# Optimization experiments

Measured on AMD Instinct MI355X. Metric: run time of the kernel, lower is better.

Reference implementation:

```python
import jax, jax.numpy as jnp
import numpy as np

N_NODES = 100000
N_EDGES = 1600000
IN_FEATS = 128
N_HIDDEN = 128
N_CLASSES = 47


def setup_inputs() -> dict:
    key = jax.random.key(0)
    ks = jax.random.split(key, 9)
    x = jax.random.normal(ks[0], (N_NODES, IN_FEATS), dtype=jnp.float32)
    src = jax.random.randint(ks[1], (N_EDGES,), 0, N_NODES, dtype=jnp.int32)
    dst = jax.random.randint(ks[2], (N_EDGES,), 0, N_NODES, dtype=jnp.int32)
    s = 0.05
    return {
        "x": x, "src": src, "dst": dst,
        "Ws0": jax.random.normal(ks[3], (IN_FEATS, N_HIDDEN), jnp.float32) * s,
        "Wn0": jax.random.normal(ks[4], (IN_FEATS, N_HIDDEN), jnp.float32) * s,
        "b0": jnp.zeros((N_HIDDEN,), jnp.float32),
        "Ws1": jax.random.normal(ks[5], (N_HIDDEN, N_HIDDEN), jnp.float32) * s,
        "Wn1": jax.random.normal(ks[6], (N_HIDDEN, N_HIDDEN), jnp.float32) * s,
        "b1": jnp.zeros((N_HIDDEN,), jnp.float32),
        "Ws2": jax.random.normal(ks[7], (N_HIDDEN, N_CLASSES), jnp.float32) * s,
        "Wn2": jax.random.normal(ks[8], (N_HIDDEN, N_CLASSES), jnp.float32) * s,
        "b2": jnp.zeros((N_CLASSES,), jnp.float32),
    }


def _sage_layer(h, src, dst, inv_deg, Ws, Wn, b):
    # weighted (w=1) mean aggregation over in-neighbors: sum(h[src]) / in_degree
    msg = h[src]  # [E, d] irregular gather
    neigh = jax.ops.segment_sum(msg, dst, num_segments=N_NODES) * inv_deg[:, None]
    # DGL SAGEConv 'mean': fc_self(h_self) + fc_neigh(h_neigh), bias on self branch
    return h @ Ws + neigh @ Wn + b


def reference(x, src, dst, Ws0, Wn0, b0, Ws1, Wn1, b1, Ws2, Wn2, b2):
    deg = jax.ops.segment_sum(jnp.ones_like(dst, dtype=x.dtype), dst, num_segments=N_NODES)
    inv_deg = 1.0 / jnp.maximum(deg, 1.0)
    h = _sage_layer(x, src, dst, inv_deg, Ws0, Wn0, b0)
    h = jax.nn.relu(h)  # dropout is identity (eval / p=0)
    h = _sage_layer(h, src, dst, inv_deg, Ws1, Wn1, b1)
    h = jax.nn.relu(h)
    h = _sage_layer(h, src, dst, inv_deg, Ws2, Wn2, b2)
    return jax.nn.log_softmax(h, axis=-1)
```

## Files before the change

### kernel.cpp

```cpp
#include <hip/hip_runtime.h>
#include <hip/hip_bf16.h>

#define NN 100000
#define NE 1600000
#define F 128
#define NCLS 47

#define NPB 256
#define BUCKETS 391
#define ABLK 512
#define ACHUNK (NE / ABLK)

typedef __attribute__((ext_vector_type(8))) short short8;
typedef __attribute__((ext_vector_type(8))) unsigned short u16x8;
typedef __attribute__((ext_vector_type(4))) float f32x4;

#define MFMA16(A, B, C) __builtin_amdgcn_mfma_f32_16x16x32_bf16(A, B, C, 0, 0, 0)

__device__ __forceinline__ unsigned short b16(float f) {
    unsigned int u = __builtin_bit_cast(unsigned int, f);
    unsigned int r = u + 0x7FFFu + ((u >> 16) & 1u);
    return (unsigned short)(r >> 16);
}
__device__ __forceinline__ float bflo(unsigned int u) { return __builtin_bit_cast(float, u << 16); }
__device__ __forceinline__ float bfhi(unsigned int u) { return __builtin_bit_cast(float, u & 0xFFFF0000u); }

__global__ void __launch_bounds__(256) k_bhist(const int* __restrict__ dst,
                                               int* __restrict__ bucket_cnt) {
    __shared__ int hist[BUCKETS];
    const int t = threadIdx.x;
    for (int i = t; i < BUCKETS; i += 256) hist[i] = 0;
    __syncthreads();
    const int e0 = blockIdx.x * ACHUNK;
    for (int i = t; i < ACHUNK; i += 256) atomicAdd(&hist[dst[e0 + i] >> 8], 1);
    __syncthreads();
    for (int i = t; i < BUCKETS; i += 256)
        if (hist[i]) atomicAdd(&bucket_cnt[i], hist[i]);
}

__global__ void k_bscan(const int* __restrict__ bucket_cnt, int* __restrict__ bucket_off,
                        int* __restrict__ cursor) {
    const int lane = threadIdx.x & 63;
    int run = 0;
#pragma unroll
    for (int c = 0; c < 7; c++) {
        int idx = c * 64 + lane;
        int v = (idx < BUCKETS) ? bucket_cnt[idx] : 0;
        int s = v;
#pragma unroll
        for (int off = 1; off < 64; off <<= 1) {
            int n = __shfl_up(s, off);
            if (lane >= off) s += n;
        }
        int excl = run + s - v;
        if (idx <= BUCKETS) {
            bucket_off[idx] = excl;
            cursor[idx] = excl;
        }
        run += __shfl(s, 63);
    }
}

__global__ void __launch_bounds__(256) k_bscatter(const int* __restrict__ src,
                                                  const int* __restrict__ dst,
                                                  int* __restrict__ cursor,
                                                  int2* __restrict__ ebuf) {
    __shared__ int hist[BUCKETS];
    __shared__ int base[BUCKETS];
    __shared__ int rank[BUCKETS];
    const int t = threadIdx.x;
    for (int i = t; i < BUCKETS; i += 256) {
        hist[i] = 0;
        rank[i] = 0;
    }
    __syncthreads();
    const int e0 = blockIdx.x * ACHUNK;
    for (int i = t; i < ACHUNK; i += 256) atomicAdd(&hist[dst[e0 + i] >> 8], 1);
    __syncthreads();
    for (int i = t; i < BUCKETS; i += 256) {
        int h = hist[i];
        base[i] = h ? atomicAdd(&cursor[i], h) : 0;
    }
    __syncthreads();
    for (int i = t; i < ACHUNK; i += 256) {
        int s = src[e0 + i];
        int d = dst[e0 + i];
        int b = d >> 8;
        int r = atomicAdd(&rank[b], 1);
        ebuf[base[b] + r] = make_int2(s, d);
    }
}

__global__ void __launch_bounds__(256) k_bcsr(const int2* __restrict__ ebuf,
                                              const int* __restrict__ bucket_off,
                                              int* __restrict__ row_off,
                                              float* __restrict__ inv_deg,
                                              int* __restrict__ col) {
    __shared__ int cnt[NPB];
    __shared__ int ro[NPB];
    __shared__ int wsum[4];
    const int t = threadIdx.x, lane = t & 63, wid = t >> 6;
    cnt[t] = 0;
    __syncthreads();
    const int e0 = bucket_off[blockIdx.x], e1 = bucket_off[blockIdx.x + 1];
    for (int i = e0 + t; i < e1; i += 256) atomicAdd(&cnt[ebuf[i].y & 255], 1);
    __syncthreads();
    int v = cnt[t];
    int run = v;
#pragma unroll
    for (int off = 1; off < 64; off <<= 1) {
        int n = __shfl_up(run, off);
        if (lane >= off) run += n;
    }
    if (lane == 63) wsum[wid] = run;
    __syncthreads();
    int woff = e0;
#pragma unroll
    for (int wv = 0; wv < 4; wv++)
        if (wv < wid) woff += wsum[wv];
    int excl = woff + run - v;
    int node = (blockIdx.x << 8) + t;
    if (node < NN) {
        row_off[node] = excl;
        inv_deg[node] = 1.0f / fmaxf((float)v, 1.0f);
    }
    if (blockIdx.x == BUCKETS - 1 && t == 0) row_off[NN] = NE;
    ro[t] = excl;
    cnt[t] = 0;
    __syncthreads();
    for (int i = e0 + t; i < e1; i += 256) {
        int2 e = ebuf[i];
        int d = e.y & 255;
        int p = atomicAdd(&cnt[d], 1);
        col[ro[d] + p] = e.x;
    }
}

__global__ void k_cvt(const float* __restrict__ x, unsigned short* __restrict__ xb) {
    int t = blockIdx.x * blockDim.x + threadIdx.x;
    if (t >= NN * F / 8) return;
    const float4* x4 = (const float4*)x;
    float4 a = x4[t * 2], b = x4[t * 2 + 1];
    u16x8 o;
    o[0] = b16(a.x); o[1] = b16(a.y); o[2] = b16(a.z); o[3] = b16(a.w);
    o[4] = b16(b.x); o[5] = b16(b.y); o[6] = b16(b.z); o[7] = b16(b.w);
    ((u16x8*)xb)[t] = o;
}

__global__ void k_zpad(unsigned short* __restrict__ xb, unsigned short* __restrict__ h1b,
                       unsigned short* __restrict__ hw2b) {
    int t = threadIdx.x;
    xb[(size_t)NN * F + t] = 0;
    h1b[(size_t)NN * F + t] = 0;
    if (t < 64) hw2b[(size_t)NN * 64 + t] = 0;
}

__global__ void k_pack_all(const float* __restrict__ Ws0, const float* __restrict__ Wn0,
                           const float* __restrict__ Ws1, const float* __restrict__ Wn1,
                           const float* __restrict__ Ws2, const float* __restrict__ Wn2,
                           unsigned short* __restrict__ wp) {
    int idx = blockIdx.x * blockDim.x + threadIdx.x;
    if (idx >= 77824) return;
    const float* W;
    int base, ncols;
    if (idx < 65536) {
        int m = idx >> 14;
        W = (m == 0) ? Ws0 : (m == 1) ? Wn0 : (m == 2) ? Ws1 : Wn1;
        base = m << 14;
        ncols = 128;
    } else {
        int m = (idx - 65536) / 6144;
        W = m ? Wn2 : Ws2;
        base = 65536 + m * 6144;
        ncols = NCLS;
    }
    int li = idx - base;
    int nt = li >> 11;
    int r = li & 2047;
    int kk = r >> 9;
    int r2 = r & 511;
    int lane = r2 >> 3;
    int j = r2 & 7;
    int k = kk * 32 + ((lane >> 4) << 3) + j;
    int n = nt * 16 + (lane & 15);
    float v = (n < ncols) ? W[k * ncols + n] : 0.f;
    wp[idx] = b16(v);
}

__global__ void __launch_bounds__(256) k_aggb(const uint4* __restrict__ h4,
                                              const int* __restrict__ row_off,
                                              const int* __restrict__ col,
                                              const float* __restrict__ inv_deg,
                                              uint4* __restrict__ a4) {
    int node = (blockIdx.x * blockDim.x + threadIdx.x) >> 6;
    int lane = threadIdx.x & 63;
    if (node >= NN) return;
    int b = row_off[node], e = row_off[node + 1];
    int deg = e - b;
    const int g = lane >> 4, fl = lane & 15;
    float acc[8];
#pragma unroll
    for (int i = 0; i < 8; i++) acc[i] = 0.f;
    for (int base = 0; base < deg; base += 64) {
        int cnt = deg - base;
        if (cnt > 64) cnt = 64;
        int myc = col[b + base + (lane < cnt ? lane : 0)];
        for (int jj = 0; jj < cnt; jj += 16) {
            uint4 u[4];
#pragma unroll
            for (int k2 = 0; k2 < 4; k2++) {
                int r = jj + k2 * 4 + g;
                int c = __shfl(myc, r);
                c = (r < cnt) ? c : NN;
                u[k2] = h4[(size_t)(unsigned)c * 16u + fl];
            }
#pragma unroll
            for (int k2 = 0; k2 < 4; k2++) {
                uint4 v = u[k2];
                acc[0] += bflo(v.x); acc[1] += bfhi(v.x);
                acc[2] += bflo(v.y); acc[3] += bfhi(v.y);
                acc[4] += bflo(v.z); acc[5] += bfhi(v.z);
                acc[6] += bflo(v.w); acc[7] += bfhi(v.w);
            }
        }
    }
#pragma unroll
    for (int i = 0; i < 8; i++) {
        acc[i] += __shfl_xor(acc[i], 16);
        acc[i] += __shfl_xor(acc[i], 32);
    }
    if (g == 0) {
        float s = inv_deg[node];
        uint4 o;
        o.x = (unsigned)b16(acc[0] * s) | ((unsigned)b16(acc[1] * s) << 16);
        o.y = (unsigned)b16(acc[2] * s) | ((unsigned)b16(acc[3] * s) << 16);
        o.z = (unsigned)b16(acc[4] * s) | ((unsigned)b16(acc[5] * s) << 16);
        o.w = (unsigned)b16(acc[6] * s) | ((unsigned)b16(acc[7] * s) << 16);
        a4[(size_t)node * 16 + fl] = o;
    }
}

__global__ void __launch_bounds__(256) k_agg48(const uint4* __restrict__ hw4,
                                               const int* __restrict__ row_off,
                                               const int* __restrict__ col,
                                               const float* __restrict__ inv_deg,
                                               float4* __restrict__ aggf4) {
    int node = (blockIdx.x * blockDim.x + threadIdx.x) >> 6;
    int lane = threadIdx.x & 63;
    if (node >= NN) return;
    int b = row_off[node], e = row_off[node + 1];
    int deg = e - b;
    const int g = lane >> 3, fl = lane & 7;
    float acc[8];
#pragma unroll
    for (int i = 0; i < 8; i++) acc[i] = 0.f;
    for (int base = 0; base < deg; base += 64) {
        int cnt = deg - base;
        if (cnt > 64) cnt = 64;
        int myc = col[b + base + (lane < cnt ? lane : 0)];
        for (int jj = 0; jj < cnt; jj += 16) {
            uint4 u[2];
#pragma unroll
            for (int k2 = 0; k2 < 2; k2++) {
                int r = jj + k2 * 8 + g;
                int c = __shfl(myc, r);
                c = (r < cnt) ? c : NN;
                u[k2] = hw4[(size_t)(unsigned)c * 8u + fl];
            }
#pragma unroll
            for (int k2 = 0; k2 < 2; k2++) {
                uint4 v = u[k2];
                acc[0] += bflo(v.x); acc[1] += bfhi(v.x);
                acc[2] += bflo(v.y); acc[3] += bfhi(v.y);
                acc[4] += bflo(v.z); acc[5] += bfhi(v.z);
                acc[6] += bflo(v.w); acc[7] += bfhi(v.w);
            }
        }
    }
#pragma unroll
    for (int i = 0; i < 8; i++) {
        acc[i] += __shfl_xor(acc[i], 8);
        acc[i] += __shfl_xor(acc[i], 16);
        acc[i] += __shfl_xor(acc[i], 32);
    }
    if (lane < 8) {
        float s = inv_deg[node];
        float4 o0 = make_float4(acc[0] * s, acc[1] * s, acc[2] * s, acc[3] * s);
        float4 o1 = make_float4(acc[4] * s, acc[5] * s, acc[6] * s, acc[7] * s);
        aggf4[(size_t)node * 16 + fl * 2] = o0;
        aggf4[(size_t)node * 16 + fl * 2 + 1] = o1;
    }
}

template <bool RELU>
__global__ void __launch_bounds__(256) k_layer(const unsigned short* __restrict__ hb,
                                               const unsigned short* __restrict__ ab,
                                               const unsigned short* __restrict__ wps,
                                               const unsigned short* __restrict__ wpn,
                                               const float* __restrict__ bias,
                                               unsigned short* __restrict__ outb) {
    const int wid = threadIdx.x >> 6, lane = threadIdx.x & 63;
    const int tile0 = blockIdx.x * 64;
    const short8* ws8 = (const short8*)wps;
    const short8* wn8 = (const short8*)wpn;
    short8 wf[2][2][4];
#pragma unroll
    for (int t = 0; t < 2; t++) {
        int nt = 2 * wid + t;
#pragma unroll
        for (int kk = 0; kk < 4; kk++) {
            wf[0][t][kk] = ws8[(nt * 4 + kk) * 64 + lane];
            wf[1][t][kk] = wn8[(nt * 4 + kk) * 64 + lane];
        }
    }
    const int rb = lane & 15, kq = lane >> 4;
    float bv[2];
#pragma unroll
    for (int t = 0; t < 2; t++) bv[t] = bias[(2 * wid + t) * 16 + rb];
    const short8* h8 = (const short8*)hb;
    const short8* a8 = (const short8*)ab;
    f32x4 zero = {0.f, 0.f, 0.f, 0.f};
    f32x4 acc[4][2];
#pragma unroll
    for (int m = 0; m < 4; m++)
#pragma unroll
        for (int t = 0; t < 2; t++) acc[m][t] = zero;
#pragma unroll
    for (int kk = 0; kk < 4; kk++) {
#pragma unroll
        for (int m = 0; m < 4; m++) {
            int row = tile0 + m * 16 + rb;
            int rc = row < NN ? row : NN - 1;
            int idx = rc * 16 + kk * 4 + kq;
            short8 af = h8[idx];
            short8 gf = a8[idx];
            acc[m][0] = MFMA16(af, wf[0][0][kk], acc[m][0]);
            acc[m][1] = MFMA16(af, wf[0][1][kk], acc[m][1]);
            acc[m][0] = MFMA16(gf, wf[1][0][kk], acc[m][0]);
            acc[m][1] = MFMA16(gf, wf[1][1][kk], acc[m][1]);
        }
    }
#pragma unroll
    for (int m = 0; m < 4; m++) {
#pragma unroll
        for (int reg = 0; reg < 4; reg++) {
            int row = tile0 + m * 16 + kq * 4 + reg;
            if (row < NN) {
#pragma unroll
                for (int t = 0; t < 2; t++) {
                    float v = acc[m][t][reg] + bv[t];
                    if (RELU) v = fmaxf(v, 0.f);
                    outb[(size_t)row * F + (2 * wid + t) * 16 + rb] = b16(v);
                }
            }
        }
    }
}

__global__ void __launch_bounds__(512) k_nmul(const unsigned short* __restrict__ hb,
                                              const unsigned short* __restrict__ wpn,
                                              unsigned short* __restrict__ hw) {
    const int wid = threadIdx.x >> 6, lane = threadIdx.x & 63;
    const int R0 = blockIdx.x * 128 + wid * 16;
    const short8* wn8 = (const short8*)wpn;
    short8 wf[3][4];
#pragma unroll
    for (int nt = 0; nt < 3; nt++)
#pragma unroll
        for (int kk = 0; kk < 4; kk++) wf[nt][kk] = wn8[(nt * 4 + kk) * 64 + lane];
    const int rb = lane & 15, kq = lane >> 4;
    const short8* h8 = (const short8*)hb;
    f32x4 zero = {0.f, 0.f, 0.f, 0.f};
    f32x4 acc[3] = {zero, zero, zero};
    int rowr = R0 + rb;
    int rc = rowr < NN ? rowr : NN - 1;
#pragma unroll
    for (int kk = 0; kk < 4; kk++) {
        short8 af = h8[rc * 16 + kk * 4 + kq];
#pragma unroll
        for (int nt = 0; nt < 3; nt++) acc[nt] = MFMA16(af, wf[nt][kk], acc[nt]);
    }
#pragma unroll
    for (int reg = 0; reg < 4; reg++) {
        int row = R0 + kq * 4 + reg;
        if (row < NN) {
#pragma unroll
            for (int nt = 0; nt < 3; nt++)
                hw[(size_t)row * 64 + nt * 16 + rb] = b16(acc[nt][reg]);
        }
    }
}

__global__ void __launch_bounds__(512) k_out2(const unsigned short* __restrict__ hb,
                                              const float* __restrict__ aggf,
                                              const unsigned short* __restrict__ wps,
                                              const float* __restrict__ bias,
                                              float* __restrict__ out) {
    const int wid = threadIdx.x >> 6, lane = threadIdx.x & 63;
    const int R0 = blockIdx.x * 128 + wid * 16;
    const short8* ws8 = (const short8*)wps;
    short8 wf[3][4];
#pragma unroll
    for (int nt = 0; nt < 3; nt++)
#pragma unroll
        for (int kk = 0; kk < 4; kk++) wf[nt][kk] = ws8[(nt * 4 + kk) * 64 + lane];
    const int rb = lane & 15, kq = lane >> 4;
    float bv[3];
    bool valid[3];
#pragma unroll
    for (int nt = 0; nt < 3; nt++) {
        int c = nt * 16 + rb;
        valid[nt] = c < NCLS;
        bv[nt] = valid[nt] ? bias[c] : 0.f;
    }
    const short8* h8 = (const short8*)hb;
    f32x4 zero = {0.f, 0.f, 0.f, 0.f};
    f32x4 acc[3] = {zero, zero, zero};
    int rowr = R0 + rb;
    int rc = rowr < NN ? rowr : NN - 1;
#pragma unroll
    for (int kk = 0; kk < 4; kk++) {
        short8 af = h8[rc * 16 + kk * 4 + kq];
#pragma unroll
        for (int nt = 0; nt < 3; nt++) acc[nt] = MFMA16(af, wf[nt][kk], acc[nt]);
    }
#pragma unroll
    for (int reg = 0; reg < 4; reg++) {
        int row = R0 + kq * 4 + reg;
        int rc2 = row < NN ? row : NN - 1;
        float v[3];
        float mx = -1e30f;
#pragma unroll
        for (int nt = 0; nt < 3; nt++) {
            float av = aggf[(size_t)rc2 * 64 + nt * 16 + rb];
            v[nt] = acc[nt][reg] + av + bv[nt];
            if (valid[nt]) mx = fmaxf(mx, v[nt]);
        }
        for (int off = 1; off < 16; off <<= 1) mx = fmaxf(mx, __shfl_xor(mx, off));
        float s = 0.f;
#pragma unroll
        for (int nt = 0; nt < 3; nt++)
            if (valid[nt]) s += expf(v[nt] - mx);
        for (int off = 1; off < 16; off <<= 1) s += __shfl_xor(s, off);
        float L = mx + logf(s);
        if (row < NN) {
#pragma unroll
            for (int nt = 0; nt < 3; nt++)
                if (valid[nt]) out[(size_t)row * NCLS + nt * 16 + rb] = v[nt] - L;
        }
    }
}

extern "C" void kernel_launch(void* const* d_in, const int* in_sizes, int n_in,
                              void* d_out, int out_size, void* d_ws, size_t ws_size,
                              hipStream_t stream) {
    (void)in_sizes; (void)n_in; (void)out_size; (void)ws_size;
    const float* x = (const float*)d_in[0];
    const int* src = (const int*)d_in[1];
    const int* dst = (const int*)d_in[2];
    const float* Ws0 = (const float*)d_in[3];
    const float* Wn0 = (const float*)d_in[4];
    const float* b0 = (const float*)d_in[5];
    const float* Ws1 = (const float*)d_in[6];
    const float* Wn1 = (const float*)d_in[7];
    const float* b1 = (const float*)d_in[8];
    const float* Ws2 = (const float*)d_in[9];
    const float* Wn2 = (const float*)d_in[10];
    const float* b2 = (const float*)d_in[11];
    float* out = (float*)d_out;

    char* w = (char*)d_ws;
    size_t off = 0;
    auto alloc = [&](size_t bytes) -> char* {
        char* p = w + off;
        off = (off + bytes + 255) & ~(size_t)255;
        return p;
    };
    int* row_off = (int*)alloc((size_t)(NN + 1) * 4);
    int* col = (int*)alloc((size_t)NE * 4);
    float* inv_deg = (float*)alloc((size_t)NN * 4);
    int* bucket_cnt = (int*)alloc((size_t)(BUCKETS + 1) * 4);
    int* bucket_off = (int*)alloc((size_t)(BUCKETS + 1) * 4);
    int* bcursor = (int*)alloc((size_t)(BUCKETS + 1) * 4);
    int2* ebuf = (int2*)alloc((size_t)NE * 8 + 256);
    unsigned short* xb = (unsigned short*)alloc((size_t)(NN + 1) * F * 2);
    unsigned short* aggb = (unsigned short*)alloc((size_t)NN * F * 2);
    unsigned short* h1b = (unsigned short*)alloc((size_t)(NN + 1) * F * 2);
    unsigned short* h2b = (unsigned short*)alloc((size_t)NN * F * 2);
    unsigned short* wp = (unsigned short*)alloc((size_t)77824 * 2);

    unsigned short* hw2b = (unsigned short*)ebuf;
    float* agg2f = (float*)aggb;

    hipMemsetAsync(bucket_cnt, 0, (size_t)(BUCKETS + 1) * 4, stream);

    k_bhist<<<ABLK, 256, 0, stream>>>(dst, bucket_cnt);
    k_bscan<<<1, 64, 0, stream>>>(bucket_cnt, bucket_off, bcursor);
    k_bscatter<<<ABLK, 256, 0, stream>>>(src, dst, bcursor, ebuf);
    k_bcsr<<<BUCKETS, 256, 0, stream>>>(ebuf, bucket_off, row_off, inv_deg, col);

    k_cvt<<<(NN * F / 8 + 255) / 256, 256, 0, stream>>>(x, xb);
    k_pack_all<<<(77824 + 255) / 256, 256, 0, stream>>>(Ws0, Wn0, Ws1, Wn1, Ws2, Wn2, wp);

    unsigned short* wS0 = wp;
    unsigned short* wN0 = wp + 16384;
    unsigned short* wS1 = wp + 32768;
    unsigned short* wN1 = wp + 49152;
    unsigned short* wS2 = wp + 65536;
    unsigned short* wN2 = wp + 71680;

    const int AGG_B = NN * 64 / 256;
    const int LYR_B = (NN + 63) / 64;
    const int OUT_B = (NN + 127) / 128;

    k_zpad<<<1, 128, 0, stream>>>(xb, h1b, hw2b);

    k_aggb<<<AGG_B, 256, 0, stream>>>((const uint4*)xb, row_off, col, inv_deg, (uint4*)aggb);
    k_layer<true><<<LYR_B, 256, 0, stream>>>(xb, aggb, wS0, wN0, b0, h1b);
    k_aggb<<<AGG_B, 256, 0, stream>>>((const uint4*)h1b, row_off, col, inv_deg, (uint4*)aggb);
    k_layer<true><<<LYR_B, 256, 0, stream>>>(h1b, aggb, wS1, wN1, b1, h2b);
    k_nmul<<<OUT_B, 512, 0, stream>>>(h2b, wN2, hw2b);
    k_agg48<<<AGG_B, 256, 0, stream>>>((const uint4*)hw2b, row_off, col, inv_deg,
                                       (float4*)agg2f);
    k_out2<<<OUT_B, 512, 0, stream>>>(h2b, agg2f, wS2, b2, out);
}
```

Baseline: 325.7 us.

## Split feature halves across XCDs, pack edge buffer, store final aggregate as bf16

The 128-wide aggregation kernel now processes each node twice, once per 64-feature half. Block indices are mapped so that the four XCDs in one half of the chip gather only one half of the feature rows. The intent is to shrink the working set each XCD's L2 must hold and so reduce gather misses. The bucket-scatter edge buffer packs src and the low 8 bits of dst into one 32-bit word instead of an int2, halving that traffic; this relies on src fitting in 24 bits. The layer-2 neighbour aggregate is also written as bf16 instead of fp32, which cuts bytes moved but loses some precision.

```diff
diff --git a/kernel.cpp b/kernel.cpp
--- a/kernel.cpp
+++ b/kernel.cpp
@@ -64,7 +64,7 @@
 __global__ void __launch_bounds__(256) k_bscatter(const int* __restrict__ src,
                                                   const int* __restrict__ dst,
                                                   int* __restrict__ cursor,
-                                                  int2* __restrict__ ebuf) {
+                                                  unsigned int* __restrict__ ebuf) {
     __shared__ int hist[BUCKETS];
     __shared__ int base[BUCKETS];
     __shared__ int rank[BUCKETS];
@@ -83,15 +83,15 @@
     }
     __syncthreads();
     for (int i = t; i < ACHUNK; i += 256) {
-        int s = src[e0 + i];
+        unsigned int s = (unsigned int)src[e0 + i];
         int d = dst[e0 + i];
         int b = d >> 8;
         int r = atomicAdd(&rank[b], 1);
-        ebuf[base[b] + r] = make_int2(s, d);
-    }
-}
-
-__global__ void __launch_bounds__(256) k_bcsr(const int2* __restrict__ ebuf,
+        ebuf[base[b] + r] = s | ((unsigned int)(d & 255) << 24);
+    }
+}
+
+__global__ void __launch_bounds__(256) k_bcsr(const unsigned int* __restrict__ ebuf,
                                               const int* __restrict__ bucket_off,
                                               int* __restrict__ row_off,
                                               float* __restrict__ inv_deg,
@@ -103,7 +103,7 @@
     cnt[t] = 0;
     __syncthreads();
     const int e0 = bucket_off[blockIdx.x], e1 = bucket_off[blockIdx.x + 1];
-    for (int i = e0 + t; i < e1; i += 256) atomicAdd(&cnt[ebuf[i].y & 255], 1);
+    for (int i = e0 + t; i < e1; i += 256) atomicAdd(&cnt[ebuf[i] >> 24], 1);
     __syncthreads();
     int v = cnt[t];
     int run = v;
@@ -129,10 +129,10 @@
     cnt[t] = 0;
     __syncthreads();
     for (int i = e0 + t; i < e1; i += 256) {
-        int2 e = ebuf[i];
-        int d = e.y & 255;
+        unsigned int e = ebuf[i];
+        int d = e >> 24;
         int p = atomicAdd(&cnt[d], 1);
-        col[ro[d] + p] = e.x;
+        col[ro[d] + p] = (int)(e & 0xFFFFFFu);
     }
 }
 
@@ -187,17 +187,22 @@
     wp[idx] = b16(v);
 }
 
-__global__ void __launch_bounds__(256) k_aggb(const uint4* __restrict__ h4,
-                                              const int* __restrict__ row_off,
-                                              const int* __restrict__ col,
-                                              const float* __restrict__ inv_deg,
-                                              uint4* __restrict__ a4) {
-    int node = (blockIdx.x * blockDim.x + threadIdx.x) >> 6;
-    int lane = threadIdx.x & 63;
+__global__ void __launch_bounds__(256) k_aggbh(const uint4* __restrict__ h4,
+                                               const int* __restrict__ row_off,
+                                               const int* __restrict__ col,
+                                               const float* __restrict__ inv_deg,
+                                               uint4* __restrict__ a4) {
+    const int bI = blockIdx.x;
+    const int xcd = bI & 7;
+    const int half = xcd >> 2;
+    const int bh = (bI >> 3) * 4 + (xcd & 3);
+    const int wid = threadIdx.x >> 6, lane = threadIdx.x & 63;
+    const int node = bh * 4 + wid;
     if (node >= NN) return;
+    const int hoff = half * 8;
     int b = row_off[node], e = row_off[node + 1];
     int deg = e - b;
-    const int g = lane >> 4, fl = lane & 15;
+    const int g = lane >> 3, fl = lane & 7;
     float acc[8];
 #pragma unroll
     for (int i = 0; i < 8; i++) acc[i] = 0.f;
@@ -206,16 +211,16 @@
         if (cnt > 64) cnt = 64;
         int myc = col[b + base + (lane < cnt ? lane : 0)];
         for (int jj = 0; jj < cnt; jj += 16) {
-            uint4 u[4];
-#pragma unroll
-            for (int k2 = 0; k2 < 4; k2++) {
-                int r = jj + k2 * 4 + g;
+            uint4 u[2];
+#pragma unroll
+            for (int k2 = 0; k2 < 2; k2++) {
+                int r = jj + k2 * 8 + g;
                 int c = __shfl(myc, r);
                 c = (r < cnt) ? c : NN;
-                u[k2] = h4[(size_t)(unsigned)c * 16u + fl];
+                u[k2] = h4[(size_t)(unsigned)c * 16u + hoff + fl];
             }
 #pragma unroll
-            for (int k2 = 0; k2 < 4; k2++) {
+            for (int k2 = 0; k2 < 2; k2++) {
                 uint4 v = u[k2];
                 acc[0] += bflo(v.x); acc[1] += bfhi(v.x);
                 acc[2] += bflo(v.y); acc[3] += bfhi(v.y);
@@ -226,17 +231,18 @@
     }
 #pragma unroll
     for (int i = 0; i < 8; i++) {
+        acc[i] += __shfl_xor(acc[i], 8);
         acc[i] += __shfl_xor(acc[i], 16);
         acc[i] += __shfl_xor(acc[i], 32);
     }
-    if (g == 0) {
+    if (lane < 8) {
         float s = inv_deg[node];
         uint4 o;
         o.x = (unsigned)b16(acc[0] * s) | ((unsigned)b16(acc[1] * s) << 16);
         o.y = (unsigned)b16(acc[2] * s) | ((unsigned)b16(acc[3] * s) << 16);
         o.z = (unsigned)b16(acc[4] * s) | ((unsigned)b16(acc[5] * s) << 16);
         o.w = (unsigned)b16(acc[6] * s) | ((unsigned)b16(acc[7] * s) << 16);
-        a4[(size_t)node * 16 + fl] = o;
+        a4[(size_t)node * 16 + hoff + fl] = o;
     }
 }
 
@@ -244,7 +250,7 @@
                                                const int* __restrict__ row_off,
                                                const int* __restrict__ col,
                                                const float* __restrict__ inv_deg,
-                                               float4* __restrict__ aggf4) {
+                                               uint4* __restrict__ aggh4) {
     int node = (blockIdx.x * blockDim.x + threadIdx.x) >> 6;
     int lane = threadIdx.x & 63;
     if (node >= NN) return;
@@ -285,10 +291,12 @@
     }
     if (lane < 8) {
         float s = inv_deg[node];
-        float4 o0 = make_float4(acc[0] * s, acc[1] * s, acc[2] * s, acc[3] * s);
-        float4 o1 = make_float4(acc[4] * s, acc[5] * s, acc[6] * s, acc[7] * s);
-        aggf4[(size_t)node * 16 + fl * 2] = o0;
-        aggf4[(size_t)node * 16 + fl * 2 + 1] = o1;
+        uint4 o;
+        o.x = (unsigned)b16(acc[0] * s) | ((unsigned)b16(acc[1] * s) << 16);
+        o.y = (unsigned)b16(acc[2] * s) | ((unsigned)b16(acc[3] * s) << 16);
+        o.z = (unsigned)b16(acc[4] * s) | ((unsigned)b16(acc[5] * s) << 16);
+        o.w = (unsigned)b16(acc[6] * s) | ((unsigned)b16(acc[7] * s) << 16);
+        aggh4[(size_t)node * 8 + fl] = o;
     }
 }
 
@@ -392,7 +400,7 @@
 }
 
 __global__ void __launch_bounds__(512) k_out2(const unsigned short* __restrict__ hb,
-                                              const float* __restrict__ aggf,
+                                              const unsigned short* __restrict__ aggh,
                                               const unsigned short* __restrict__ wps,
                                               const float* __restrict__ bias,
                                               float* __restrict__ out) {
@@ -432,7 +440,8 @@
         float mx = -1e30f;
 #pragma unroll
         for (int nt = 0; nt < 3; nt++) {
-            float av = aggf[(size_t)rc2 * 64 + nt * 16 + rb];
+            float av = __builtin_bit_cast(
+                float, (unsigned)aggh[(size_t)rc2 * 64 + nt * 16 + rb] << 16);
             v[nt] = acc[nt][reg] + av + bv[nt];
             if (valid[nt]) mx = fmaxf(mx, v[nt]);
         }
@@ -482,7 +491,7 @@
     int* bucket_cnt = (int*)alloc((size_t)(BUCKETS + 1) * 4);
     int* bucket_off = (int*)alloc((size_t)(BUCKETS + 1) * 4);
     int* bcursor = (int*)alloc((size_t)(BUCKETS + 1) * 4);
-    int2* ebuf = (int2*)alloc((size_t)NE * 8 + 256);
+    unsigned int* ebuf = (unsigned int*)alloc((size_t)(NN + 1) * 64 * 2);
     unsigned short* xb = (unsigned short*)alloc((size_t)(NN + 1) * F * 2);
     unsigned short* aggb = (unsigned short*)alloc((size_t)NN * F * 2);
     unsigned short* h1b = (unsigned short*)alloc((size_t)(NN + 1) * F * 2);
@@ -490,7 +499,7 @@
     unsigned short* wp = (unsigned short*)alloc((size_t)77824 * 2);
 
     unsigned short* hw2b = (unsigned short*)ebuf;
-    float* agg2f = (float*)aggb;
+    unsigned short* aggh = aggb;
 
     hipMemsetAsync(bucket_cnt, 0, (size_t)(BUCKETS + 1) * 4, stream);
 
@@ -509,18 +518,19 @@
     unsigned short* wS2 = wp + 65536;
     unsigned short* wN2 = wp + 71680;
 
+    const int AGGH_B = 50000;
     const int AGG_B = NN * 64 / 256;
     const int LYR_B = (NN + 63) / 64;
     const int OUT_B = (NN + 127) / 128;
 
     k_zpad<<<1, 128, 0, stream>>>(xb, h1b, hw2b);
 
-    k_aggb<<<AGG_B, 256, 0, stream>>>((const uint4*)xb, row_off, col, inv_deg, (uint4*)aggb);
+    k_aggbh<<<AGGH_B, 256, 0, stream>>>((const uint4*)xb, row_off, col, inv_deg, (uint4*)aggb);
     k_layer<true><<<LYR_B, 256, 0, stream>>>(xb, aggb, wS0, wN0, b0, h1b);
-    k_aggb<<<AGG_B, 256, 0, stream>>>((const uint4*)h1b, row_off, col, inv_deg, (uint4*)aggb);
+    k_aggbh<<<AGGH_B, 256, 0, stream>>>((const uint4*)h1b, row_off, col, inv_deg, (uint4*)aggb);
     k_layer<true><<<LYR_B, 256, 0, stream>>>(h1b, aggb, wS1, wN1, b1, h2b);
     k_nmul<<<OUT_B, 512, 0, stream>>>(h2b, wN2, hw2b);
     k_agg48<<<AGG_B, 256, 0, stream>>>((const uint4*)hw2b, row_off, col, inv_deg,
-                                       (float4*)agg2f);
-    k_out2<<<OUT_B, 512, 0, stream>>>(h2b, agg2f, wS2, b2, out);
-}
+                                       (uint4*)aggh);
+    k_out2<<<OUT_B, 512, 0, stream>>>(h2b, aggh, wS2, b2, out);
+}
```

Measured after the change: 360.1 us. 1.11x slower.
